# Optimization experiments

Hardware: AMD Instinct MI355X
Metric: run time of the kernel (lower is better)

The kernel has to match this reference:

```python
import jax, jax.numpy as jnp
import numpy as np

NH, WS, SS = 8, 7, 3  # num_heads, window_size, shift_size
EPS = 1e-5


def _rel_pos_index(ws):
    coords = np.stack(np.meshgrid(np.arange(ws), np.arange(ws), indexing='ij'))
    coords = coords.reshape(2, -1)                      # [2, L]
    rel = coords[:, :, None] - coords[:, None, :]       # [2, L, L]
    rel = rel.transpose(1, 2, 0) + (ws - 1)
    return rel[..., 0] * (2 * ws - 1) + rel[..., 1]     # [L, L] int


def _attn_mask(H, W, ws, ss):
    # region labels for shifted-window masking (torchvision semantics)
    img = np.zeros((H, W))
    slices = (slice(0, -ws), slice(-ws, -ss), slice(-ss, None))
    cnt = 0
    for hs in slices:
        for wsl in slices:
            img[hs, wsl] = cnt
            cnt += 1
    win = img.reshape(H // ws, ws, W // ws, ws).transpose(0, 2, 1, 3).reshape(-1, ws * ws)
    mask = (win[:, None, :] != win[:, :, None]).astype(np.float32) * (-100.0)
    return mask  # [nWin, L, L]


def _layernorm(x, gamma, beta):
    mu = jnp.mean(x, axis=-1, keepdims=True)
    var = jnp.mean(jnp.square(x - mu), axis=-1, keepdims=True)
    return (x - mu) * jax.lax.rsqrt(var + EPS) * gamma + beta


def _swin_attention(x, qkv_w, qkv_b, proj_w, proj_b, rpb_table):
    B, H, W, C = x.shape
    HD = C // NH
    L = WS * WS
    nH, nW = H // WS, W // WS
    # cyclic shift
    xs = jnp.roll(x, shift=(-SS, -SS), axis=(1, 2))
    # window partition -> [B*nWin, L, C]
    xw = xs.reshape(B, nH, WS, nW, WS, C).transpose(0, 1, 3, 2, 4, 5).reshape(B * nH * nW, L, C)
    qkv = jnp.einsum('nlc,dc->nld', xw, qkv_w) + qkv_b
    qkv = qkv.reshape(-1, L, 3, NH, HD).transpose(2, 0, 3, 1, 4)  # [3, N, h, L, d]
    q, k, v = qkv[0] * (HD ** -0.5), qkv[1], qkv[2]
    attn = jnp.einsum('nhid,nhjd->nhij', q, k)  # [N, h, L, L]
    bias = rpb_table[jnp.asarray(_rel_pos_index(WS))]  # [L, L, h]
    attn = attn + bias.transpose(2, 0, 1)[None]
    mask = jnp.asarray(_attn_mask(H, W, WS, SS))  # [nWin, L, L]
    nwin = nH * nW
    attn = attn.reshape(B, nwin, NH, L, L) + mask[None, :, None]
    attn = jax.nn.softmax(attn.reshape(-1, NH, L, L), axis=-1)
    out = jnp.einsum('nhij,nhjd->nhid', attn, v).transpose(0, 2, 1, 3).reshape(-1, L, C)
    out = jnp.einsum('nlc,dc->nld', out, proj_w) + proj_b
    # reverse windows and shift
    out = out.reshape(B, nH, nW, WS, WS, C).transpose(0, 1, 3, 2, 4, 5).reshape(B, H, W, C)
    return jnp.roll(out, shift=(SS, SS), axis=(1, 2))


def setup_inputs() -> dict:
    key = jax.random.key(0)
    ks = jax.random.split(key, 8)
    B, H, W, C = 32, 56, 56, 256
    F = 4 * C
    s = 0.02
    return {
        'x': jax.random.normal(ks[0], (B, H, W, C), jnp.float32),
        'qkv_w': jax.random.normal(ks[1], (3 * C, C), jnp.float32) * s,
        'qkv_b': jnp.zeros((3 * C,), jnp.float32),
        'proj_w': jax.random.normal(ks[2], (C, C), jnp.float32) * s,
        'proj_b': jnp.zeros((C,), jnp.float32),
        'rpb_table': jax.random.normal(ks[3], ((2 * WS - 1) ** 2, NH), jnp.float32) * s,
        'gamma1': jnp.ones((C,), jnp.float32),
        'beta1': jnp.zeros((C,), jnp.float32),
        'w1': jax.random.normal(ks[4], (C, F), jnp.float32) * s,
        'b1': jax.random.normal(ks[5], (F,), jnp.float32) * 1e-6,
        'w2': jax.random.normal(ks[6], (F, C), jnp.float32) * s,
        'b2': jax.random.normal(ks[7], (C,), jnp.float32) * 1e-6,
        'gamma2': jnp.ones((C,), jnp.float32),
        'beta2': jnp.zeros((C,), jnp.float32),
    }


def reference(x, qkv_w, qkv_b, proj_w, proj_b, rpb_table, gamma1, beta1, w1, b1, w2, b2, gamma2, beta2):
    # post-norm residual block: x + norm1(attn(x)); x + norm2(mlp(x))
    a = _swin_attention(x, qkv_w, qkv_b, proj_w, proj_b, rpb_table)
    x = x + _layernorm(a, gamma1, beta1)
    h = jax.nn.gelu(jnp.einsum('bhwc,cf->bhwf', x, w1) + b1, approximate=False)
    m = jnp.einsum('bhwf,fc->bhwc', h, w2) + b2
    x = x + _layernorm(m, gamma2, beta2)
    return x
```

## Files before the change

kernel.cpp:

```cpp
#include <hip/hip_runtime.h>
#include <hip/hip_bf16.h>


typedef unsigned short ushort_t;
typedef short bf16x8 __attribute__((ext_vector_type(8)));
typedef float f32x4 __attribute__((ext_vector_type(4)));

#define WAITV0 asm volatile("s_waitcnt vmcnt(0)" ::: "memory")
#define WAITL0 asm volatile("s_waitcnt lgkmcnt(0)" ::: "memory")
#define BAR    __builtin_amdgcn_s_barrier()

__device__ __forceinline__ float bf2f(unsigned short u) {
    union { unsigned int i; float f; } x; x.i = ((unsigned int)u) << 16; return x.f;
}
__device__ __forceinline__ unsigned short f2bf(float f) {
    union { float f; unsigned int i; } x; x.f = f;
    unsigned int r = x.i + 0x7fffu + ((x.i >> 16) & 1u);
    return (unsigned short)(r >> 16);
}
__device__ __forceinline__ bf16x8 pack8(float4 a, float4 b) {
    bf16x8 r;
    r[0] = (short)f2bf(a.x); r[1] = (short)f2bf(a.y);
    r[2] = (short)f2bf(a.z); r[3] = (short)f2bf(a.w);
    r[4] = (short)f2bf(b.x); r[5] = (short)f2bf(b.y);
    r[6] = (short)f2bf(b.z); r[7] = (short)f2bf(b.w);
    return r;
}
__device__ __forceinline__ void gl_lds16(const ushort_t* g, ushort_t* l) {
    __builtin_amdgcn_global_load_lds((const __attribute__((address_space(1))) void*)g,
                                     (__attribute__((address_space(3))) void*)l, 16, 0, 0);
}
__device__ __forceinline__ float gelu_f(float v) {
    float s = v * 0.70710678118654752f;
    float ax = fabsf(s);
    float t = __builtin_amdgcn_rcpf(1.0f + 0.3275911f * ax);
    float poly = ((((1.061405429f * t - 1.453152027f) * t + 1.421413741f) * t
                   - 0.284496736f) * t + 0.254829592f) * t;
    float y = 1.0f - poly * __expf(-ax * ax);
    float e = (s < 0.f) ? -y : y;
    return 0.5f * v * (1.0f + e);
}

__device__ __forceinline__ long swin_src_off(int m) {
    int n = m / 49, l = m - n * 49;
    int b = n >> 6, win = n & 63;
    int wh = win >> 3, ww = win & 7;
    int i = l / 7, j = l - i * 7;
    int hs = wh * 7 + i + 3; if (hs >= 56) hs -= 56;
    int ws = ww * 7 + j + 3; if (ws >= 56) ws -= 56;
    return ((long)(b * 56 + hs) * 56 + ws) * 256;
}

template<int SRCT>
__global__ __launch_bounds__(256)
void convW(const float* __restrict__ src, ushort_t* __restrict__ dst, int N, int kshift)
{
    int idx = blockIdx.x * 256 + threadIdx.x;
    int kk = idx & ((1 << kshift) - 1), nn = idx >> kshift;
    float v = SRCT ? src[(long)kk * N + nn] : src[idx];
    dst[idx] = f2bf(v);
}

template<int ACT, int AMODE, int NCOLS>
__global__ __launch_bounds__(512)
void gemmW(const void* __restrict__ Av, const ushort_t* __restrict__ W,
           const float* __restrict__ bias, ushort_t* __restrict__ C,
           int M, int N, int K)
{
    __shared__ ushort_t As[2][128 * 32];
    __shared__ ushort_t Bs[2][256 * 32];
    const int t = threadIdx.x, lane = t & 63, w = t >> 6;
    const int cpx = gridDim.x >> 3;
    const int wg = (blockIdx.x & 7) * cpx + (blockIdx.x >> 3);
    const int row0 = (wg / NCOLS) * 128, col0 = (wg % NCOLS) * 256;
    const int wm = (w >> 2) * 64, wn = (w & 3) * 64;

    const int ra = t >> 2, sa = ((t & 3) ^ ((ra >> 1) & 3)) * 8;
    const ushort_t* ag = nullptr;
    const float* axr = nullptr;
    if (AMODE == 0) ag = (const ushort_t*)Av + (long)(row0 + ra) * K + sa;
    else            axr = (const float*)Av + swin_src_off(row0 + ra) + sa;

    const int ub0 = t, ub1 = t + 512;
    const int rb0 = ub0 >> 2, sb0 = ((ub0 & 3) ^ ((rb0 >> 1) & 3)) * 8;
    const int rb1 = ub1 >> 2, sb1 = ((ub1 & 3) ^ ((rb1 >> 1) & 3)) * 8;
    const ushort_t* bg0 = W + (long)(col0 + rb0) * K + sb0;
    const ushort_t* bg1 = W + (long)(col0 + rb1) * K + sb1;

    int offA[4], offB[4];
    #pragma unroll
    for (int i = 0; i < 4; i++) {
        int r2 = wm + i * 16 + (lane & 15);
        offA[i] = r2 * 32 + (((lane >> 4) ^ ((r2 >> 1) & 3)) * 8);
        int r3 = wn + i * 16 + (lane & 15);
        offB[i] = r3 * 32 + (((lane >> 4) ^ ((r3 >> 1) & 3)) * 8);
    }

    f32x4 acc[4][4] = {};
    if (AMODE == 0) {
        gl_lds16(ag, &As[0][t * 8]);
    } else {
        float4 va = *(const float4*)axr, vb = *(const float4*)(axr + 4);
        *(bf16x8*)&As[0][t * 8] = pack8(va, vb);
    }
    gl_lds16(bg0, &Bs[0][ub0 * 8]);
    gl_lds16(bg1, &Bs[0][ub1 * 8]);
    WAITV0; if (AMODE == 1) { WAITL0; } BAR;

    const int nk = K >> 5;
    for (int kt = 0; kt < nk - 1; kt++) {
        const int cur = kt & 1, nxt = cur ^ 1, k1 = (kt + 1) * 32;
        float4 va, vb;
        if (AMODE == 1) {
            va = *(const float4*)(axr + k1);
            vb = *(const float4*)(axr + k1 + 4);
        } else {
            gl_lds16(ag + k1, &As[nxt][t * 8]);
        }
        gl_lds16(bg0 + k1, &Bs[nxt][ub0 * 8]);
        gl_lds16(bg1 + k1, &Bs[nxt][ub1 * 8]);
        bf16x8 af[4], bw[4];
        #pragma unroll
        for (int i = 0; i < 4; i++) {
            af[i] = *(const bf16x8*)&As[cur][offA[i]];
            bw[i] = *(const bf16x8*)&Bs[cur][offB[i]];
        }
        #pragma unroll
        for (int mi = 0; mi < 4; mi++)
            #pragma unroll
            for (int ni = 0; ni < 4; ni++)
                acc[mi][ni] = __builtin_amdgcn_mfma_f32_16x16x32_bf16(af[mi], bw[ni], acc[mi][ni], 0, 0, 0);
        if (AMODE == 1)
            *(bf16x8*)&As[nxt][t * 8] = pack8(va, vb);
        WAITV0; if (AMODE == 1) { WAITL0; } BAR;
    }
    {
        const int cur = (nk - 1) & 1;
        bf16x8 af[4], bw[4];
        #pragma unroll
        for (int i = 0; i < 4; i++) {
            af[i] = *(const bf16x8*)&As[cur][offA[i]];
            bw[i] = *(const bf16x8*)&Bs[cur][offB[i]];
        }
        #pragma unroll
        for (int mi = 0; mi < 4; mi++)
            #pragma unroll
            for (int ni = 0; ni < 4; ni++)
                acc[mi][ni] = __builtin_amdgcn_mfma_f32_16x16x32_bf16(af[mi], bw[ni], acc[mi][ni], 0, 0, 0);
    }
    #pragma unroll
    for (int mi = 0; mi < 4; mi++)
        #pragma unroll
        for (int ni = 0; ni < 4; ni++) {
            const int c = col0 + wn + ni * 16 + (lane & 15);
            const float bv = bias[c];
            #pragma unroll
            for (int r = 0; r < 4; r++) {
                const int rr = row0 + wm + mi * 16 + (lane >> 4) * 4 + r;
                float v = acc[mi][ni][r] + bv;
                if (ACT) v = gelu_f(v);
                C[(long)rr * N + c] = f2bf(v);
            }
        }
}

__global__ __launch_bounds__(64)
void attn_mfma(const ushort_t* __restrict__ qkv, const float* __restrict__ rpb,
               ushort_t* __restrict__ out)
{
    __shared__ ushort_t v_t[32 * 72];
    __shared__ ushort_t p_lds[64 * 72];
    __shared__ float bias_s[169];

    const int blk = blockIdx.x;
    const int n = blk >> 3, h = blk & 7;
    const int l = threadIdx.x;
    const long wbase = (long)n * 49 * 768 + h * 32;
    const float scale = 0.17677669529663687f;

    {
        int j = min(l, 48);
        const ushort_t* vr = qkv + wbase + (long)j * 768 + 512;
        #pragma unroll
        for (int c = 0; c < 4; c++) {
            bf16x8 vv = *(const bf16x8*)(vr + c * 8);
            #pragma unroll
            for (int e = 0; e < 8; e++) v_t[(c * 8 + e) * 72 + l] = (ushort_t)vv[e];
        }
    }
    for (int idx = l; idx < 169; idx += 64) bias_s[idx] = rpb[idx * 8 + h];
    __syncthreads();

    f32x4 s[4][4] = {};
    {
        bf16x8 aq[4], bk[4];
        #pragma unroll
        for (int mt = 0; mt < 4; mt++) {
            int i = min(mt * 16 + (l & 15), 48);
            aq[mt] = *(const bf16x8*)(qkv + wbase + (long)i * 768 + (l >> 4) * 8);
        }
        #pragma unroll
        for (int nt = 0; nt < 4; nt++) {
            int j = min(nt * 16 + (l & 15), 48);
            bk[nt] = *(const bf16x8*)(qkv + wbase + (long)j * 768 + 256 + (l >> 4) * 8);
        }
        #pragma unroll
        for (int mt = 0; mt < 4; mt++)
            #pragma unroll
            for (int nt = 0; nt < 4; nt++)
                s[mt][nt] = __builtin_amdgcn_mfma_f32_16x16x32_bf16(aq[mt], bk[nt], s[mt][nt], 0, 0, 0);
    }

    const int win = n & 63, wh = win >> 3, ww = win & 7;
    int yj[4], xj[4], regj[4]; bool jv[4];
    #pragma unroll
    for (int nt = 0; nt < 4; nt++) {
        int j = nt * 16 + (l & 15);
        jv[nt] = (j <= 48);
        int jc = min(j, 48);
        yj[nt] = jc / 7; xj[nt] = jc - yj[nt] * 7;
        int hs = wh * 7 + yj[nt], wsx = ww * 7 + xj[nt];
        regj[nt] = (hs < 49 ? 0 : (hs < 53 ? 1 : 2)) * 3 + (wsx < 49 ? 0 : (wsx < 53 ? 1 : 2));
    }
    float rinv[4][4];
    #pragma unroll
    for (int mt = 0; mt < 4; mt++) {
        #pragma unroll
        for (int r = 0; r < 4; r++) {
            int i = mt * 16 + (l >> 4) * 4 + r;
            int ic = min(i, 48);
            int yi = ic / 7, xi = ic - yi * 7;
            int hs = wh * 7 + yi, wsx = ww * 7 + xi;
            int regi = (hs < 49 ? 0 : (hs < 53 ? 1 : 2)) * 3 + (wsx < 49 ? 0 : (wsx < 53 ? 1 : 2));
            float val[4];
            #pragma unroll
            for (int nt = 0; nt < 4; nt++) {
                float v = s[mt][nt][r] * scale + bias_s[(yi - yj[nt] + 6) * 13 + (xi - xj[nt] + 6)];
                if (regi != regj[nt]) v -= 100.f;
                val[nt] = jv[nt] ? v : -1e30f;
            }
            float mx = fmaxf(fmaxf(val[0], val[1]), fmaxf(val[2], val[3]));
            #pragma unroll
            for (int off = 1; off <= 8; off <<= 1) mx = fmaxf(mx, __shfl_xor(mx, off));
            float sum = 0.f;
            #pragma unroll
            for (int nt = 0; nt < 4; nt++) { val[nt] = __expf(val[nt] - mx); sum += val[nt]; }
            #pragma unroll
            for (int off = 1; off <= 8; off <<= 1) sum += __shfl_xor(sum, off);
            rinv[mt][r] = 1.0f / sum;
            #pragma unroll
            for (int nt = 0; nt < 4; nt++)
                p_lds[i * 72 + nt * 16 + (l & 15)] = f2bf(val[nt]);
        }
    }
    __syncthreads();

    f32x4 o[4][2] = {};
    #pragma unroll
    for (int ks = 0; ks < 2; ks++) {
        bf16x8 pa[4], vb[2];
        #pragma unroll
        for (int mt = 0; mt < 4; mt++)
            pa[mt] = *(const bf16x8*)&p_lds[(mt * 16 + (l & 15)) * 72 + ks * 32 + (l >> 4) * 8];
        #pragma unroll
        for (int nt = 0; nt < 2; nt++)
            vb[nt] = *(const bf16x8*)&v_t[(nt * 16 + (l & 15)) * 72 + ks * 32 + (l >> 4) * 8];
        #pragma unroll
        for (int mt = 0; mt < 4; mt++)
            #pragma unroll
            for (int nt = 0; nt < 2; nt++)
                o[mt][nt] = __builtin_amdgcn_mfma_f32_16x16x32_bf16(pa[mt], vb[nt], o[mt][nt], 0, 0, 0);
    }
    #pragma unroll
    for (int mt = 0; mt < 4; mt++)
        #pragma unroll
        for (int r = 0; r < 4; r++) {
            int i = mt * 16 + (l >> 4) * 4 + r;
            if (i < 49) {
                float rs = rinv[mt][r];
                #pragma unroll
                for (int nt = 0; nt < 2; nt++) {
                    int d = nt * 16 + (l & 15);
                    out[((long)n * 49 + i) * 256 + h * 32 + d] = f2bf(o[mt][nt][r] * rs);
                }
            }
        }
}

__global__ __launch_bounds__(512)
void projln1(const ushort_t* __restrict__ A, const ushort_t* __restrict__ W,
             const float* __restrict__ pb, const float* __restrict__ x,
             const float* __restrict__ gamma, const float* __restrict__ beta,
             ushort_t* __restrict__ x1b)
{
    __shared__ ushort_t As[2][128 * 32];
    __shared__ ushort_t Bs[2][256 * 32];
    __shared__ float red_s[128][4];
    __shared__ float red_ss[128][4];
    __shared__ int srow_s[128];
    const int t = threadIdx.x, lane = t & 63, w = t >> 6;
    const int row0 = blockIdx.x * 128;
    const int wm = (w >> 2) * 64, wn = (w & 3) * 64;

    if (t < 128) srow_s[t] = (int)(swin_src_off(row0 + t) >> 8);

    const int ra0 = t >> 2, sa0 = ((t & 3) ^ ((ra0 >> 1) & 3)) * 8;
    const ushort_t* ag = A + (long)(row0 + ra0) * 256 + sa0;
    const int ub0 = t, ub1 = t + 512;
    const int rb0 = ub0 >> 2, sb0 = ((ub0 & 3) ^ ((rb0 >> 1) & 3)) * 8;
    const int rb1 = ub1 >> 2, sb1 = ((ub1 & 3) ^ ((rb1 >> 1) & 3)) * 8;
    const ushort_t* bg0 = W + (long)rb0 * 256 + sb0;
    const ushort_t* bg1 = W + (long)rb1 * 256 + sb1;

    int offA[4], offB[4];
    #pragma unroll
    for (int i = 0; i < 4; i++) {
        int ra = wm + i * 16 + (lane & 15);
        offA[i] = ra * 32 + (((lane >> 4) ^ ((ra >> 1) & 3)) * 8);
        int rb = wn + i * 16 + (lane & 15);
        offB[i] = rb * 32 + (((lane >> 4) ^ ((rb >> 1) & 3)) * 8);
    }

    f32x4 acc[4][4] = {};
    gl_lds16(ag, &As[0][t * 8]);
    gl_lds16(bg0, &Bs[0][ub0 * 8]); gl_lds16(bg1, &Bs[0][ub1 * 8]);
    WAITV0; BAR;
    for (int kt = 0; kt < 7; kt++) {
        const int cur = kt & 1, nxt = cur ^ 1, k1 = (kt + 1) * 32;
        gl_lds16(ag + k1, &As[nxt][t * 8]);
        gl_lds16(bg0 + k1, &Bs[nxt][ub0 * 8]); gl_lds16(bg1 + k1, &Bs[nxt][ub1 * 8]);
        bf16x8 af[4], bw[4];
        #pragma unroll
        for (int i = 0; i < 4; i++) {
            af[i] = *(const bf16x8*)&As[cur][offA[i]];
            bw[i] = *(const bf16x8*)&Bs[cur][offB[i]];
        }
        #pragma unroll
        for (int mi = 0; mi < 4; mi++)
            #pragma unroll
            for (int ni = 0; ni < 4; ni++)
                acc[mi][ni] = __builtin_amdgcn_mfma_f32_16x16x32_bf16(af[mi], bw[ni], acc[mi][ni], 0, 0, 0);
        WAITV0; BAR;
    }
    {
        bf16x8 af[4], bw[4];
        #pragma unroll
        for (int i = 0; i < 4; i++) {
            af[i] = *(const bf16x8*)&As[1][offA[i]];
            bw[i] = *(const bf16x8*)&Bs[1][offB[i]];
        }
        #pragma unroll
        for (int mi = 0; mi < 4; mi++)
            #pragma unroll
            for (int ni = 0; ni < 4; ni++)
                acc[mi][ni] = __builtin_amdgcn_mfma_f32_16x16x32_bf16(af[mi], bw[ni], acc[mi][ni], 0, 0, 0);
    }

    float pbv[4], g1v[4], be1v[4];
    #pragma unroll
    for (int ni = 0; ni < 4; ni++) {
        int col = wn + ni * 16 + (lane & 15);
        pbv[ni] = pb[col]; g1v[ni] = gamma[col]; be1v[ni] = beta[col];
    }
    #pragma unroll
    for (int mi = 0; mi < 4; mi++)
        #pragma unroll
        for (int rr = 0; rr < 4; rr++) {
            float s = 0.f, ss = 0.f;
            #pragma unroll
            for (int ni = 0; ni < 4; ni++) {
                float v = acc[mi][ni][rr] + pbv[ni];
                acc[mi][ni][rr] = v; s += v; ss += v * v;
            }
            #pragma unroll
            for (int off = 1; off <= 8; off <<= 1) { s += __shfl_xor(s, off); ss += __shfl_xor(ss, off); }
            if ((lane & 15) == 0) {
                int r = wm + mi * 16 + (lane >> 4) * 4 + rr;
                red_s[r][w & 3] = s; red_ss[r][w & 3] = ss;
            }
        }
    __syncthreads();
    #pragma unroll
    for (int mi = 0; mi < 4; mi++)
        #pragma unroll
        for (int rr = 0; rr < 4; rr++) {
            const int r = wm + mi * 16 + (lane >> 4) * 4 + rr;
            const float s = red_s[r][0] + red_s[r][1] + red_s[r][2] + red_s[r][3];
            const float ss = red_ss[r][0] + red_ss[r][1] + red_ss[r][2] + red_ss[r][3];
            const float mu = s * (1.0f / 256.0f);
            const float rstd = rsqrtf(ss * (1.0f / 256.0f) - mu * mu + 1e-5f);
            const long sp = srow_s[r];
            #pragma unroll
            for (int ni = 0; ni < 4; ni++) {
                int col = wn + ni * 16 + (lane & 15);
                float o = x[sp * 256 + col] + (acc[mi][ni][rr] - mu) * rstd * g1v[ni] + be1v[ni];
                x1b[sp * 256 + col] = f2bf(o);
            }
        }
}

__global__ __launch_bounds__(256)
void mlp2ln2(const ushort_t* __restrict__ A, const ushort_t* __restrict__ W,
             const float* __restrict__ pb, const ushort_t* __restrict__ x1res,
             const float* __restrict__ gamma, const float* __restrict__ beta,
             float* __restrict__ out)
{
    __shared__ ushort_t As[2][64 * 32];
    __shared__ ushort_t Bs[2][256 * 32];
    __shared__ float red_s[64][4];
    __shared__ float red_ss[64][4];
    const int t = threadIdx.x, lane = t & 63, w = t >> 6;
    const int row0 = blockIdx.x * 64;
    const int wn = w * 64;

    const int ra0 = t >> 2, sa0 = ((t & 3) ^ ((ra0 >> 1) & 3)) * 8;
    const ushort_t* ag = A + (long)(row0 + ra0) * 1024 + sa0;
    const ushort_t* bg[4];
    int ub[4];
    #pragma unroll
    for (int i = 0; i < 4; i++) {
        ub[i] = t + i * 256;
        int rb = ub[i] >> 2, sb = ((ub[i] & 3) ^ ((rb >> 1) & 3)) * 8;
        bg[i] = W + (long)rb * 1024 + sb;
    }

    int offA[4], offB[4];
    #pragma unroll
    for (int i = 0; i < 4; i++) {
        int ra = i * 16 + (lane & 15);
        offA[i] = ra * 32 + (((lane >> 4) ^ ((ra >> 1) & 3)) * 8);
        int rb = wn + i * 16 + (lane & 15);
        offB[i] = rb * 32 + (((lane >> 4) ^ ((rb >> 1) & 3)) * 8);
    }

    f32x4 acc[4][4] = {};
    gl_lds16(ag, &As[0][t * 8]);
    #pragma unroll
    for (int i = 0; i < 4; i++) gl_lds16(bg[i], &Bs[0][ub[i] * 8]);
    WAITV0; BAR;
    for (int kt = 0; kt < 31; kt++) {
        const int cur = kt & 1, nxt = cur ^ 1, k1 = (kt + 1) * 32;
        gl_lds16(ag + k1, &As[nxt][t * 8]);
        #pragma unroll
        for (int i = 0; i < 4; i++) gl_lds16(bg[i] + k1, &Bs[nxt][ub[i] * 8]);
        bf16x8 af[4], bw[4];
        #pragma unroll
        for (int i2 = 0; i2 < 4; i2++) {
            af[i2] = *(const bf16x8*)&As[cur][offA[i2]];
            bw[i2] = *(const bf16x8*)&Bs[cur][offB[i2]];
        }
        #pragma unroll
        for (int mi = 0; mi < 4; mi++)
            #pragma unroll
            for (int ni = 0; ni < 4; ni++)
                acc[mi][ni] = __builtin_amdgcn_mfma_f32_16x16x32_bf16(af[mi], bw[ni], acc[mi][ni], 0, 0, 0);
        WAITV0; BAR;
    }
    {
        bf16x8 af[4], bw[4];
        #pragma unroll
        for (int i2 = 0; i2 < 4; i2++) {
            af[i2] = *(const bf16x8*)&As[1][offA[i2]];
            bw[i2] = *(const bf16x8*)&Bs[1][offB[i2]];
        }
        #pragma unroll
        for (int mi = 0; mi < 4; mi++)
            #pragma unroll
            for (int ni = 0; ni < 4; ni++)
                acc[mi][ni] = __builtin_amdgcn_mfma_f32_16x16x32_bf16(af[mi], bw[ni], acc[mi][ni], 0, 0, 0);
    }
    float pbv[4], g2v[4], be2v[4];
    #pragma unroll
    for (int ni = 0; ni < 4; ni++) {
        int col = wn + ni * 16 + (lane & 15);
        pbv[ni] = pb[col]; g2v[ni] = gamma[col]; be2v[ni] = beta[col];
    }
    #pragma unroll
    for (int mi = 0; mi < 4; mi++)
        #pragma unroll
        for (int rr = 0; rr < 4; rr++) {
            float s = 0.f, ss = 0.f;
            #pragma unroll
            for (int ni = 0; ni < 4; ni++) {
                float v = acc[mi][ni][rr] + pbv[ni];
                acc[mi][ni][rr] = v; s += v; ss += v * v;
            }
            #pragma unroll
            for (int off = 1; off <= 8; off <<= 1) { s += __shfl_xor(s, off); ss += __shfl_xor(ss, off); }
            if ((lane & 15) == 0) {
                int r = mi * 16 + (lane >> 4) * 4 + rr;
                red_s[r][w] = s; red_ss[r][w] = ss;
            }
        }
    __syncthreads();
    #pragma unroll
    for (int mi = 0; mi < 4; mi++)
        #pragma unroll
        for (int rr = 0; rr < 4; rr++) {
            const int r = mi * 16 + (lane >> 4) * 4 + rr;
            const float s = red_s[r][0] + red_s[r][1] + red_s[r][2] + red_s[r][3];
            const float ss = red_ss[r][0] + red_ss[r][1] + red_ss[r][2] + red_ss[r][3];
            const float mu = s * (1.0f / 256.0f);
            const float rstd = rsqrtf(ss * (1.0f / 256.0f) - mu * mu + 1e-5f);
            const long gr = row0 + r;
            #pragma unroll
            for (int ni = 0; ni < 4; ni++) {
                int col = wn + ni * 16 + (lane & 15);
                out[gr * 256 + col] = bf2f(x1res[gr * 256 + col])
                                    + (acc[mi][ni][rr] - mu) * rstd * g2v[ni] + be2v[ni];
            }
        }
}

extern "C" void kernel_launch(void* const* d_in, const int* in_sizes, int n_in,
                              void* d_out, int out_size, void* d_ws, size_t ws_size,
                              hipStream_t stream) {
    const float* x      = (const float*)d_in[0];
    const float* qkv_w  = (const float*)d_in[1];
    const float* qkv_b  = (const float*)d_in[2];
    const float* proj_w = (const float*)d_in[3];
    const float* proj_b = (const float*)d_in[4];
    const float* rpb    = (const float*)d_in[5];
    const float* gamma1 = (const float*)d_in[6];
    const float* beta1  = (const float*)d_in[7];
    const float* w1     = (const float*)d_in[8];
    const float* b1     = (const float*)d_in[9];
    const float* w2     = (const float*)d_in[10];
    const float* b2     = (const float*)d_in[11];
    const float* gamma2 = (const float*)d_in[12];
    const float* beta2  = (const float*)d_in[13];
    float* outf = (float*)d_out;

    ushort_t* attnout = (ushort_t*)d_out;

    char* ws = (char*)d_ws;
    ushort_t* qkvb  = (ushort_t*)ws;
    ushort_t* hbuf  = (ushort_t*)ws;
    ushort_t* x1b   = (ushort_t*)(ws + 154140672ULL);
    ushort_t* wqkvb = (ushort_t*)(ws + 205520896ULL);
    ushort_t* wprojb= (ushort_t*)(ws + 205914112ULL);
    ushort_t* w1t   = (ushort_t*)(ws + 206045184ULL);
    ushort_t* w2t   = (ushort_t*)(ws + 206569472ULL);

    const int M = 100352, MC = 50176;
    dim3 blk(256);
    convW<0><<<dim3(768),  blk, 0, stream>>>(qkv_w,  wqkvb,  768,  8);
    convW<0><<<dim3(256),  blk, 0, stream>>>(proj_w, wprojb, 256,  8);
    convW<1><<<dim3(1024), blk, 0, stream>>>(w1,     w1t,    1024, 8);
    convW<1><<<dim3(1024), blk, 0, stream>>>(w2,     w2t,    256, 10);
    gemmW<0, 1, 3><<<dim3(2352), dim3(512), 0, stream>>>(x, wqkvb, qkv_b, qkvb, M, 768, 256);
    attn_mfma<<<dim3(16384), dim3(64), 0, stream>>>(qkvb, rpb, attnout);
    projln1<<<dim3(784), dim3(512), 0, stream>>>(attnout, wprojb, proj_b, x,
                                                 gamma1, beta1, x1b);
    for (int c2 = 0; c2 < 2; c2++) {
        const long off = (long)c2 * MC * 256;
        gemmW<1, 0, 4><<<dim3(1568), dim3(512), 0, stream>>>(x1b + off, w1t, b1, hbuf, MC, 1024, 256);
        mlp2ln2<<<dim3(784), blk, 0, stream>>>(hbuf, w2t, b2, x1b + off,
                                               gamma2, beta2, outf + off);
    }
}
```

Baseline: 537.7 us.

## Triple-buffer LDS tiles in GEMM kernels with two-stage-ahead prefetch

Converts the double-buffered K-loop in gemmW, projln1 and mlp2ln2 to a three-stage LDS ring, issuing global-to-LDS loads two tiles ahead. It waits with partial vmcnt counts so only the oldest tile must land before the barrier, instead of draining all outstanding loads each iteration. This aims to hide global memory latency behind MFMA work. In exchange it uses 1.5x the LDS per block, which can lower occupancy, and it relies on correct hand-counted vmcnt values.

```diff
diff --git a/kernel.cpp b/kernel.cpp
--- a/kernel.cpp
+++ b/kernel.cpp
@@ -7,6 +7,9 @@
 typedef float f32x4 __attribute__((ext_vector_type(4)));
 
 #define WAITV0 asm volatile("s_waitcnt vmcnt(0)" ::: "memory")
+#define WAITV3 asm volatile("s_waitcnt vmcnt(3)" ::: "memory")
+#define WAITV4 asm volatile("s_waitcnt vmcnt(4)" ::: "memory")
+#define WAITV5 asm volatile("s_waitcnt vmcnt(5)" ::: "memory")
 #define WAITL0 asm volatile("s_waitcnt lgkmcnt(0)" ::: "memory")
 #define BAR    __builtin_amdgcn_s_barrier()
 
@@ -67,8 +70,9 @@
            const float* __restrict__ bias, ushort_t* __restrict__ C,
            int M, int N, int K)
 {
-    __shared__ ushort_t As[2][128 * 32];
-    __shared__ ushort_t Bs[2][256 * 32];
+    constexpr int NA = (AMODE == 1) ? 2 : 3;
+    __shared__ ushort_t As[NA * 4096];
+    __shared__ ushort_t Bs[3 * 8192];
     const int t = threadIdx.x, lane = t & 63, w = t >> 6;
     const int cpx = gridDim.x >> 3;
     const int wg = (blockIdx.x & 7) * cpx + (blockIdx.x >> 3);
@@ -97,57 +101,72 @@
     }
 
     f32x4 acc[4][4] = {};
+    float4 va0, vb0, va1, vb1;
+
     if (AMODE == 0) {
-        gl_lds16(ag, &As[0][t * 8]);
+        gl_lds16(ag,      &As[t * 8]);
+        gl_lds16(bg0,      &Bs[ub0 * 8]);
+        gl_lds16(bg1,      &Bs[ub1 * 8]);
+        gl_lds16(ag + 32, &As[4096 + t * 8]);
+        gl_lds16(bg0 + 32, &Bs[8192 + ub0 * 8]);
+        gl_lds16(bg1 + 32, &Bs[8192 + ub1 * 8]);
+        WAITV3; BAR;
     } else {
-        float4 va = *(const float4*)axr, vb = *(const float4*)(axr + 4);
-        *(bf16x8*)&As[0][t * 8] = pack8(va, vb);
-    }
-    gl_lds16(bg0, &Bs[0][ub0 * 8]);
-    gl_lds16(bg1, &Bs[0][ub1 * 8]);
-    WAITV0; if (AMODE == 1) { WAITL0; } BAR;
+        va0 = *(const float4*)axr;        vb0 = *(const float4*)(axr + 4);
+        gl_lds16(bg0,      &Bs[ub0 * 8]);
+        gl_lds16(bg1,      &Bs[ub1 * 8]);
+        va1 = *(const float4*)(axr + 32); vb1 = *(const float4*)(axr + 36);
+        gl_lds16(bg0 + 32, &Bs[8192 + ub0 * 8]);
+        gl_lds16(bg1 + 32, &Bs[8192 + ub1 * 8]);
+        WAITV4;
+        *(bf16x8*)&As[t * 8] = pack8(va0, vb0);
+        WAITL0; BAR;
+    }
 
     const int nk = K >> 5;
-    for (int kt = 0; kt < nk - 1; kt++) {
-        const int cur = kt & 1, nxt = cur ^ 1, k1 = (kt + 1) * 32;
-        float4 va, vb;
-        if (AMODE == 1) {
-            va = *(const float4*)(axr + k1);
-            vb = *(const float4*)(axr + k1 + 4);
-        } else {
-            gl_lds16(ag + k1, &As[nxt][t * 8]);
-        }
-        gl_lds16(bg0 + k1, &Bs[nxt][ub0 * 8]);
-        gl_lds16(bg1 + k1, &Bs[nxt][ub1 * 8]);
-        bf16x8 af[4], bw[4];
-        #pragma unroll
-        for (int i = 0; i < 4; i++) {
-            af[i] = *(const bf16x8*)&As[cur][offA[i]];
-            bw[i] = *(const bf16x8*)&Bs[cur][offB[i]];
-        }
-        #pragma unroll
-        for (int mi = 0; mi < 4; mi++)
-            #pragma unroll
-            for (int ni = 0; ni < 4; ni++)
-                acc[mi][ni] = __builtin_amdgcn_mfma_f32_16x16x32_bf16(af[mi], bw[ni], acc[mi][ni], 0, 0, 0);
-        if (AMODE == 1)
-            *(bf16x8*)&As[nxt][t * 8] = pack8(va, vb);
-        WAITV0; if (AMODE == 1) { WAITL0; } BAR;
-    }
-    {
-        const int cur = (nk - 1) & 1;
-        bf16x8 af[4], bw[4];
-        #pragma unroll
-        for (int i = 0; i < 4; i++) {
-            af[i] = *(const bf16x8*)&As[cur][offA[i]];
-            bw[i] = *(const bf16x8*)&Bs[cur][offB[i]];
-        }
-        #pragma unroll
-        for (int mi = 0; mi < 4; mi++)
-            #pragma unroll
-            for (int ni = 0; ni < 4; ni++)
-                acc[mi][ni] = __builtin_amdgcn_mfma_f32_16x16x32_bf16(af[mi], bw[ni], acc[mi][ni], 0, 0, 0);
-    }
+    int i0 = 0, i1 = 1, i2 = 2;
+    for (int kt = 0; kt < nk; kt++) {
+        const bool more = (kt + 2 < nk);
+        if (more) {
+            const int k2 = (kt + 2) * 32;
+            if (AMODE == 0) {
+                gl_lds16(ag + k2, &As[i2 * 4096 + t * 8]);
+            } else {
+                if (kt & 1) { va1 = *(const float4*)(axr + k2); vb1 = *(const float4*)(axr + k2 + 4); }
+                else        { va0 = *(const float4*)(axr + k2); vb0 = *(const float4*)(axr + k2 + 4); }
+            }
+            gl_lds16(bg0 + k2, &Bs[i2 * 8192 + ub0 * 8]);
+            gl_lds16(bg1 + k2, &Bs[i2 * 8192 + ub1 * 8]);
+        }
+        {
+            const int abase = (AMODE == 1 ? (kt & 1) : i0) * 4096;
+            const int bbase = i0 * 8192;
+            bf16x8 af[4], bw[4];
+            #pragma unroll
+            for (int i = 0; i < 4; i++) {
+                af[i] = *(const bf16x8*)&As[abase + offA[i]];
+                bw[i] = *(const bf16x8*)&Bs[bbase + offB[i]];
+            }
+            #pragma unroll
+            for (int mi = 0; mi < 4; mi++)
+                #pragma unroll
+                for (int ni = 0; ni < 4; ni++)
+                    acc[mi][ni] = __builtin_amdgcn_mfma_f32_16x16x32_bf16(af[mi], bw[ni], acc[mi][ni], 0, 0, 0);
+        }
+        if (kt < nk - 1) {
+            if (AMODE == 0) {
+                if (more) { WAITV3; } else { WAITV0; }
+            } else {
+                if (more) { WAITV4; } else { WAITV0; }
+                if (kt & 1) *(bf16x8*)&As[t * 8]        = pack8(va0, vb0);
+                else        *(bf16x8*)&As[4096 + t * 8] = pack8(va1, vb1);
+                WAITL0;
+            }
+            BAR;
+        }
+        int tmp = i0; i0 = i1; i1 = i2; i2 = tmp;
+    }
+
     #pragma unroll
     for (int mi = 0; mi < 4; mi++)
         #pragma unroll
@@ -293,8 +312,8 @@
              const float* __restrict__ gamma, const float* __restrict__ beta,
              ushort_t* __restrict__ x1b)
 {
-    __shared__ ushort_t As[2][128 * 32];
-    __shared__ ushort_t Bs[2][256 * 32];
+    __shared__ ushort_t As[3 * 4096];
+    __shared__ ushort_t Bs[3 * 8192];
     __shared__ float red_s[128][4];
     __shared__ float red_ss[128][4];
     __shared__ int srow_s[128];
@@ -322,38 +341,39 @@
     }
 
     f32x4 acc[4][4] = {};
-    gl_lds16(ag, &As[0][t * 8]);
-    gl_lds16(bg0, &Bs[0][ub0 * 8]); gl_lds16(bg1, &Bs[0][ub1 * 8]);
-    WAITV0; BAR;
-    for (int kt = 0; kt < 7; kt++) {
-        const int cur = kt & 1, nxt = cur ^ 1, k1 = (kt + 1) * 32;
-        gl_lds16(ag + k1, &As[nxt][t * 8]);
-        gl_lds16(bg0 + k1, &Bs[nxt][ub0 * 8]); gl_lds16(bg1 + k1, &Bs[nxt][ub1 * 8]);
+    gl_lds16(ag,       &As[t * 8]);
+    gl_lds16(bg0,       &Bs[ub0 * 8]);
+    gl_lds16(bg1,       &Bs[ub1 * 8]);
+    gl_lds16(ag + 32,  &As[4096 + t * 8]);
+    gl_lds16(bg0 + 32,  &Bs[8192 + ub0 * 8]);
+    gl_lds16(bg1 + 32,  &Bs[8192 + ub1 * 8]);
+    WAITV3; BAR;
+
+    int i0 = 0, i1 = 1, i2 = 2;
+    for (int kt = 0; kt < 8; kt++) {
+        const bool more = (kt + 2 < 8);
+        if (more) {
+            const int k2 = (kt + 2) * 32;
+            gl_lds16(ag + k2, &As[i2 * 4096 + t * 8]);
+            gl_lds16(bg0 + k2, &Bs[i2 * 8192 + ub0 * 8]);
+            gl_lds16(bg1 + k2, &Bs[i2 * 8192 + ub1 * 8]);
+        }
         bf16x8 af[4], bw[4];
         #pragma unroll
         for (int i = 0; i < 4; i++) {
-            af[i] = *(const bf16x8*)&As[cur][offA[i]];
-            bw[i] = *(const bf16x8*)&Bs[cur][offB[i]];
+            af[i] = *(const bf16x8*)&As[i0 * 4096 + offA[i]];
+            bw[i] = *(const bf16x8*)&Bs[i0 * 8192 + offB[i]];
         }
         #pragma unroll
         for (int mi = 0; mi < 4; mi++)
             #pragma unroll
             for (int ni = 0; ni < 4; ni++)
                 acc[mi][ni] = __builtin_amdgcn_mfma_f32_16x16x32_bf16(af[mi], bw[ni], acc[mi][ni], 0, 0, 0);
-        WAITV0; BAR;
-    }
-    {
-        bf16x8 af[4], bw[4];
-        #pragma unroll
-        for (int i = 0; i < 4; i++) {
-            af[i] = *(const bf16x8*)&As[1][offA[i]];
-            bw[i] = *(const bf16x8*)&Bs[1][offB[i]];
-        }
-        #pragma unroll
-        for (int mi = 0; mi < 4; mi++)
-            #pragma unroll
-            for (int ni = 0; ni < 4; ni++)
-                acc[mi][ni] = __builtin_amdgcn_mfma_f32_16x16x32_bf16(af[mi], bw[ni], acc[mi][ni], 0, 0, 0);
+        if (kt < 7) {
+            if (more) { WAITV3; } else { WAITV0; }
+            BAR;
+        }
+        int tmp = i0; i0 = i1; i1 = i2; i2 = tmp;
     }
 
     float pbv[4], g1v[4], be1v[4];
@@ -405,8 +425,8 @@
              const float* __restrict__ gamma, const float* __restrict__ beta,
              float* __restrict__ out)
 {
-    __shared__ ushort_t As[2][64 * 32];
-    __shared__ ushort_t Bs[2][256 * 32];
+    __shared__ ushort_t As[3 * 2048];
+    __shared__ ushort_t Bs[3 * 8192];
     __shared__ float red_s[64][4];
     __shared__ float red_ss[64][4];
     const int t = threadIdx.x, lane = t & 63, w = t >> 6;
@@ -434,41 +454,41 @@
     }
 
     f32x4 acc[4][4] = {};
-    gl_lds16(ag, &As[0][t * 8]);
-    #pragma unroll
-    for (int i = 0; i < 4; i++) gl_lds16(bg[i], &Bs[0][ub[i] * 8]);
-    WAITV0; BAR;
-    for (int kt = 0; kt < 31; kt++) {
-        const int cur = kt & 1, nxt = cur ^ 1, k1 = (kt + 1) * 32;
-        gl_lds16(ag + k1, &As[nxt][t * 8]);
-        #pragma unroll
-        for (int i = 0; i < 4; i++) gl_lds16(bg[i] + k1, &Bs[nxt][ub[i] * 8]);
+    gl_lds16(ag,      &As[t * 8]);
+    #pragma unroll
+    for (int i = 0; i < 4; i++) gl_lds16(bg[i],      &Bs[ub[i] * 8]);
+    gl_lds16(ag + 32, &As[2048 + t * 8]);
+    #pragma unroll
+    for (int i = 0; i < 4; i++) gl_lds16(bg[i] + 32, &Bs[8192 + ub[i] * 8]);
+    WAITV5; BAR;
+
+    int i0 = 0, i1 = 1, i2 = 2;
+    for (int kt = 0; kt < 32; kt++) {
+        const bool more = (kt + 2 < 32);
+        if (more) {
+            const int k2 = (kt + 2) * 32;
+            gl_lds16(ag + k2, &As[i2 * 2048 + t * 8]);
+            #pragma unroll
+            for (int i = 0; i < 4; i++) gl_lds16(bg[i] + k2, &Bs[i2 * 8192 + ub[i] * 8]);
+        }
         bf16x8 af[4], bw[4];
         #pragma unroll
-        for (int i2 = 0; i2 < 4; i2++) {
-            af[i2] = *(const bf16x8*)&As[cur][offA[i2]];
-            bw[i2] = *(const bf16x8*)&Bs[cur][offB[i2]];
+        for (int i2x = 0; i2x < 4; i2x++) {
+            af[i2x] = *(const bf16x8*)&As[i0 * 2048 + offA[i2x]];
+            bw[i2x] = *(const bf16x8*)&Bs[i0 * 8192 + offB[i2x]];
         }
         #pragma unroll
         for (int mi = 0; mi < 4; mi++)
             #pragma unroll
             for (int ni = 0; ni < 4; ni++)
                 acc[mi][ni] = __builtin_amdgcn_mfma_f32_16x16x32_bf16(af[mi], bw[ni], acc[mi][ni], 0, 0, 0);
-        WAITV0; BAR;
-    }
-    {
-        bf16x8 af[4], bw[4];
-        #pragma unroll
-        for (int i2 = 0; i2 < 4; i2++) {
-            af[i2] = *(const bf16x8*)&As[1][offA[i2]];
-            bw[i2] = *(const bf16x8*)&Bs[1][offB[i2]];
-        }
-        #pragma unroll
-        for (int mi = 0; mi < 4; mi++)
-            #pragma unroll
-            for (int ni = 0; ni < 4; ni++)
-                acc[mi][ni] = __builtin_amdgcn_mfma_f32_16x16x32_bf16(af[mi], bw[ni], acc[mi][ni], 0, 0, 0);
-    }
+        if (kt < 31) {
+            if (more) { WAITV5; } else { WAITV0; }
+            BAR;
+        }
+        int tmp = i0; i0 = i1; i1 = i2; i2 = tmp;
+    }
+
     float pbv[4], g2v[4], be2v[4];
     #pragma unroll
     for (int ni = 0; ni < 4; ni++) {
```

Measured after the change: 529.4 us. Within noise of the previous version (-1.5%).
